# Performance work log

Hardware: AMD Instinct MI355X
Metric: run time of the kernel (lower is better)

## Reference

```python
import jax, jax.numpy as jnp
from jax import lax
import numpy as np

M, CLS, K, DL, DC, DO, BD = 87, 65, 128, 128, 128, 2048, 256
B, H, W = 256, 7, 7


def _c1(x, Wt, b):
    # 1x1 Conv2d: [B,Cin,H,W] -> [B,Cout,H,W]
    return jnp.einsum('oc,bchw->bohw', Wt, x) + b[None, :, None, None]


def _pagerank(edge, v_init, p=0.85, iters=100):
    # torch: transition = adj / adj.sum(dim=1)  (broadcast divides COLUMNS by row-sums)
    n = edge.shape[0]
    Wpr = p * edge / jnp.sum(edge, axis=1)[None, :]
    s = v_init * n                                  # [B,n,1]
    coef = (1.0 - p) / n
    def body(i, xv):
        zx = coef * jnp.sum(xv, axis=1, keepdims=True)      # z_T @ x -> [B,1,1]
        return jnp.einsum('ij,bjo->bio', Wpr, xv) + s * zx
    xv = lax.fori_loop(0, iters, body, s)
    nrm = jnp.sqrt(jnp.sum(xv * xv, axis=1, keepdims=True))  # F.normalize(dim=1)
    xv = xv / jnp.maximum(nrm, 1e-12)
    return (v_init + xv).reshape(v_init.shape[0], -1)        # [B,n]


def setup_inputs() -> dict:
    key = jax.random.key(0)
    ks = jax.random.split(key, 24)
    def w(k, shape, s=0.02):
        return jax.random.normal(k, shape, jnp.float32) * s
    rng = np.random.default_rng(0)
    A = (rng.random((M, M)) < 0.08).astype(np.float32)
    A = np.maximum(A, A.T)
    np.fill_diagonal(A, 1.0)   # symmetric adjacency with self-loops (degrees > 0)
    return {
        'x': jax.random.normal(ks[0], (B, DO, H, W), jnp.float32),
        'Wb': w(ks[1], (BD, DO)), 'bb': w(ks[2], (BD,), 0.01),
        'Wfc': w(ks[3], (CLS, BD)), 'Wfc2': w(ks[4], (CLS, BD)),
        'Wo1': w(ks[5], (4 * DL, DO)), 'bo1': w(ks[6], (4 * DL,), 0.01),
        'Wo2': w(ks[7], (DL, 4 * DL)), 'bo2': w(ks[8], (DL,), 0.01),
        'Wa': w(ks[9], (M, DL)), 'ba': w(ks[10], (M,), 0.01),
        'Wps': w(ks[11], (DC, DL)), 'bps': w(ks[12], (DC,), 0.01),
        'node_p': jax.random.uniform(ks[13], (K, M), jnp.float32, -0.1, 0.1),
        'Wg': w(ks[14], (DC, DC + K)), 'bg': w(ks[15], (DC,), 0.01),
        'Wsp': w(ks[16], (DL, DC)), 'bsp': w(ks[17], (DL,), 0.01),
        'Ws': w(ks[18], (1, DC + DL)), 'bs': w(ks[19], (1,), 0.01),
        'Wox1': w(ks[20], (4 * DL, DL)), 'box1': w(ks[21], (4 * DL,), 0.01),
        'Wox2': w(ks[22], (DO, 4 * DL)), 'box2': w(ks[23], (DO,), 0.01),
        'edge': jnp.asarray(A),
    }


def reference(x, Wb, bb, Wfc, Wfc2, Wo1, bo1, Wo2, bo2, Wa, ba, Wps, bps,
              node_p, Wg, bg, Wsp, bsp, Ws, bs, Wox1, box1, Wox2, box2, edge):
    Bsz, _, hl, wl = x.shape
    HW = hl * wl

    # global pooled branch
    x_p = jnp.mean(x, axis=(2, 3))                           # [B,2048]
    features_p = x_p @ Wb.T + bb                             # [B,256]
    pre_output = features_p @ Wfc.T                          # [B,65]
    pre_score = jax.nn.softmax(lax.stop_gradient(pre_output), axis=1)

    # personalized pagerank over the semantic graph (constant wrt grads)
    v_init = jnp.concatenate(
        [jnp.zeros((Bsz, M - CLS), x.dtype), pre_score], axis=1)[:, :, None]
    v_y = lax.stop_gradient(_pagerank(edge, v_init))         # [B,87]

    # local feature reduction 2048 -> 512 -> 128
    x_l = _c1(_c1(x, Wo1, bo1), Wo2, bo2)                    # [B,128,7,7]

    a = _c1(x_l, Wa, ba).reshape(Bsz, M, HW).transpose(0, 2, 1)   # [B,HW,87]
    ps = _c1(x_l, Wps, bps).reshape(Bsz, DC, HW)                  # [B,128,HW]
    m1 = jax.nn.relu(jnp.matmul(ps, a))                           # [B,128,87]

    # replicate torch's exact (k, B*m) reshape + flat v_y broadcast
    node = jnp.broadcast_to(node_p[None], (Bsz, K, M)).reshape(K, Bsz * M)
    node = (v_y.reshape(-1) * node).reshape(Bsz, K, M)

    g = jnp.einsum('oc,bcm->bom', Wg, jnp.concatenate([node, m1], axis=1)) \
        + bg[None, :, None]                                   # [B,128,87]

    # D^-1/2 A D^-1/2 graph propagation
    Dinv = jnp.sum(edge, axis=0) ** -0.5
    edge_norm = Dinv[:, None] * edge * Dinv[None, :]
    m2 = jax.nn.relu(jnp.einsum('bcm,mn->bcn', g, edge_norm))  # [B,128,87]

    sp = jnp.einsum('oc,bcm->bom', Wsp, m2) + bsp[None, :, None]  # [B,128,87]

    # conv_s over concat(m2_expand, x_expand) is separable: avoid the
    # [B,256,HW,87] tensor entirely (1 output channel, 1x1 kernel).
    Ws1, Ws2 = Ws[0, :DC], Ws[0, DC:]
    t_node = jnp.einsum('c,bcm->bm', Ws1, m2)                  # [B,87]
    t_pix = jnp.einsum('c,bcp->bp', Ws2, x_l.reshape(Bsz, DL, HW))  # [B,HW]
    s_logits = t_node[:, :, None] + t_pix[:, None, :] + bs[0]  # [B,87,HW]
    s_att = jax.nn.softmax(s_logits, axis=1)                   # softmax over nodes

    m3 = jax.nn.relu(jnp.matmul(sp, s_att)).reshape(Bsz, DL, hl, wl)
    m3 = _c1(_c1(m3, Wox1, box1), Wox2, box2)                  # [B,2048,7,7]

    feature_aug = jnp.mean(m3, axis=(2, 3)) @ Wb.T + bb
    features = features_p + feature_aug
    outputs2 = features @ Wfc2.T
    softmax_outputs = jax.nn.softmax(outputs2, axis=1)
    return (features, outputs2, softmax_outputs, pre_output, features_p)
```

## Files before the change

### kernel.cpp

```cpp
#include <hip/hip_runtime.h>
#include <cmath>


typedef __attribute__((ext_vector_type(8))) short short8;
typedef __attribute__((ext_vector_type(4))) short s16x4;
typedef __attribute__((ext_vector_type(4))) float f32x4;

constexpr size_t OFF_W12BF = 0;
constexpr size_t OFF_T1BF  = 131072;
constexpr size_t OFF_WBBF  = 262144;
constexpr size_t OFF_XPBF  = 524288;
constexpr size_t OFF_WAPBF = 786432;
constexpr size_t OFF_WG2BF = 800768;
constexpr size_t OFF_ENPBF = 808960;
constexpr size_t OFF_B215  = 813568;
constexpr size_t OFF_B12   = 813792;
constexpr size_t OFF_WPR   = 813920;
constexpr size_t OFF_BTMP  = 821496;
constexpr size_t OFF_WC    = 823544;
constexpr size_t OFF_BC    = 856312;
constexpr size_t OFF_VY    = 856568;
constexpr size_t OFF_NT    = 878848;
constexpr size_t OFF_PART  = 901376;

__device__ __forceinline__ unsigned short f2bf(float f) {
  unsigned u = __builtin_bit_cast(unsigned, f);
  u += 0x7fffu + ((u >> 16) & 1u);
  return (unsigned short)(u >> 16);
}
__device__ __forceinline__ float bf2f(unsigned short s) {
  return __builtin_bit_cast(float, ((unsigned)s) << 16);
}

__global__ __launch_bounds__(256) void ksetup_all(
    const float* __restrict__ Wb,  const float* __restrict__ bb,
    const float* __restrict__ Wa,  const float* __restrict__ ba,
    const float* __restrict__ Wps, const float* __restrict__ bps,
    const float* __restrict__ Wg,  const float* __restrict__ edge,
    const float* __restrict__ Wo2, const float* __restrict__ Wo1,
    const float* __restrict__ Wox2,const float* __restrict__ Wox1,
    const float* __restrict__ box1,const float* __restrict__ box2,
    const float* __restrict__ bo1, const float* __restrict__ bo2,
    float* __restrict__ ws, float* __restrict__ featp)
{
  __shared__ alignas(16) short As[64*72];
  __shared__ alignas(16) short Bs[64*72];
  int blk = blockIdx.x, tid = threadIdx.x;
  if (blk < 2048) {
    int idx = blk*256 + tid;
    ((unsigned short*)(ws+OFF_WBBF))[idx] = f2bf(Wb[idx]);
  } else if (blk < 2304) {
    int idx = (blk-2048)*256 + tid;
    featp[idx] = bb[idx & 255];
  } else if (blk < 2432) {
    int idx = (blk-2304)*256 + tid;
    ws[OFF_WC + idx] = 0.f;
  } else if (blk < 2544) {
    int idx = (blk-2432)*256 + tid;
    int r = idx >> 7, c = idx & 127;
    float v;
    if (r < 128)      v = Wps[r*128 + c];
    else if (r < 215) v = Wa[(r-128)*128 + c];
    else              v = 0.f;
    ((unsigned short*)(ws+OFF_WAPBF))[idx] = f2bf(v);
  } else if (blk < 2608) {
    int idx = (blk-2544)*256 + tid;
    int o = idx >> 7, d = idx & 127;
    ((unsigned short*)(ws+OFF_WG2BF))[idx] = f2bf(Wg[o*256 + 128 + d]);
  } else if (blk < 2644) {
    int idx = (blk-2608)*256 + tid;
    int m = idx / 96, n = idx % 96;
    float v = 0.f;
    if (m < 87 && n < 87) {
      float sm = 0.f, sn = 0.f;
      for (int k = 0; k < 87; ++k) { sm += edge[k*87+m]; sn += edge[k*87+n]; }
      v = edge[m*87+n] / sqrtf(sm*sn);
    }
    ((unsigned short*)(ws+OFF_ENPBF))[idx] = f2bf(v);
  } else if (blk < 2674) {
    int idx = (blk-2644)*256 + tid;
    if (idx < 87*87) {
      int j = idx % 87;
      float rs = 0.f;
      for (int k = 0; k < 87; ++k) rs += edge[j*87+k];
      ws[OFF_WPR + idx] = 0.85f * edge[idx] / rs;
    }
  } else if (blk == 2674) {
    if (tid < 224) {
      float v = (tid < 128) ? bps[tid] : (tid < 215 ? ba[tid-128] : 0.f);
      ws[OFF_B215 + tid] = v;
    }
  } else if (blk < 2803) {
    int gb = blk - 2675;
    const float *A, *B; unsigned short* C; int lda, ldb, ldc, i0, j0;
    if (gb < 64) {
      A = Wo2; B = Wo1; C = (unsigned short*)(ws+OFF_W12BF);
      lda = 512; ldb = 2048; ldc = 2048;
      i0 = (gb & 1)*64; j0 = (gb >> 1)*64;
    } else {
      int b2 = gb - 64;
      A = Wox2; B = Wox1; C = (unsigned short*)(ws+OFF_T1BF);
      lda = 512; ldb = 128; ldc = 128;
      i0 = (b2 >> 1)*64; j0 = (b2 & 1)*64;
    }
    int w = tid >> 6, l = tid & 63, quad = l >> 4, lane16 = l & 15;
    f32x4 acc[4];
    #pragma unroll
    for (int i = 0; i < 4; ++i) acc[i] = (f32x4)(0.f);
    for (int kc = 0; kc < 512; kc += 64) {
      for (int t = tid; t < 1024; t += 256) {
        int r = t >> 4, k4 = t & 15;
        float4 v = *(const float4*)&A[(size_t)(i0+r)*lda + kc + k4*4];
        s16x4 sv; sv[0]=(short)f2bf(v.x); sv[1]=(short)f2bf(v.y); sv[2]=(short)f2bf(v.z); sv[3]=(short)f2bf(v.w);
        *(s16x4*)&As[r*72 + k4*4] = sv;
      }
      for (int t = tid; t < 1024; t += 256) {
        int kr = t >> 4, n4 = t & 15;
        float4 v = *(const float4*)&B[(size_t)(kc+kr)*ldb + j0 + n4*4];
        Bs[(n4*4+0)*72 + kr] = (short)f2bf(v.x);
        Bs[(n4*4+1)*72 + kr] = (short)f2bf(v.y);
        Bs[(n4*4+2)*72 + kr] = (short)f2bf(v.z);
        Bs[(n4*4+3)*72 + kr] = (short)f2bf(v.w);
      }
      __syncthreads();
      #pragma unroll
      for (int ks = 0; ks < 2; ++ks) {
        short8 a = *(const short8*)&As[(w*16+lane16)*72 + ks*32 + quad*8];
        #pragma unroll
        for (int nt = 0; nt < 4; ++nt) {
          short8 b8 = *(const short8*)&Bs[(nt*16+lane16)*72 + ks*32 + quad*8];
          acc[nt] = __builtin_amdgcn_mfma_f32_16x16x32_bf16(a, b8, acc[nt], 0, 0, 0);
        }
      }
      __syncthreads();
    }
    #pragma unroll
    for (int nt = 0; nt < 4; ++nt)
      #pragma unroll
      for (int r = 0; r < 4; ++r)
        C[(size_t)(i0 + w*16 + quad*4 + r)*ldc + j0 + nt*16 + lane16] = f2bf(acc[nt][r]);
  } else {
    int vb = blk - 2803;
    int w = tid >> 6, l = tid & 63;
    if (vb < 512) {
      int o = vb*4 + w;
      float s = 0.f;
      for (int h = l; h < 512; h += 64) s += Wox2[(size_t)o*512 + h] * box1[h];
      for (int off = 32; off; off >>= 1) s += __shfl_down(s, off, 64);
      if (l == 0) ws[OFF_BTMP + o] = s + box2[o];
    } else {
      int o = (vb - 512)*4 + w;
      float s = 0.f;
      for (int h = l; h < 512; h += 64) s += Wo2[(size_t)o*512 + h] * bo1[h];
      for (int off = 32; off; off >>= 1) s += __shfl_down(s, off, 64);
      if (l == 0) ws[OFF_B12 + o] = s + bo2[o];
    }
  }
}

__global__ __launch_bounds__(512, 6) void kmain5(const float* __restrict__ x,
                                                 const short* __restrict__ w12bf,
                                                 short* __restrict__ xpbf,
                                                 float* __restrict__ part)
{
  __shared__ alignas(16) short Bt[2][64*72];
  int b = blockIdx.x, q = blockIdx.y, tid = threadIdx.x;
  int w = tid >> 6, l = tid & 63;
  int quad = l >> 4, lane16 = l & 15;
  const float* xb = x + ((size_t)b*2048 + q*512)*49;

  int p4A = tid % 13, cA = tid / 13;
  int tB = tid + 512;
  int p4B = tB % 13, cB = tB / 13;
  bool hasB = (tid < 320);

  float fA[4], fB[4];
  {
    if (p4A < 12) {
      float4 v = *(const float4*)(xb + cA*49 + p4A*4);
      fA[0]=v.x; fA[1]=v.y; fA[2]=v.z; fA[3]=v.w;
    } else fA[0] = xb[cA*49 + 48];
    if (hasB) {
      if (p4B < 12) {
        float4 v = *(const float4*)(xb + cB*49 + p4B*4);
        fB[0]=v.x; fB[1]=v.y; fB[2]=v.z; fB[3]=v.w;
      } else fB[0] = xb[cB*49 + 48];
    }
  }

  f32x4 acc[4];
  #pragma unroll
  for (int i = 0; i < 4; ++i) acc[i] = (f32x4)(0.f);

  for (int kci = 0; kci < 8; ++kci) {
    short* bt = Bt[kci & 1];
    if (p4A < 12) {
      #pragma unroll
      for (int i = 0; i < 4; ++i) bt[(p4A*4+i)*72 + cA] = (short)f2bf(fA[i]);
    } else bt[48*72 + cA] = (short)f2bf(fA[0]);
    if (hasB) {
      if (p4B < 12) {
        #pragma unroll
        for (int i = 0; i < 4; ++i) bt[(p4B*4+i)*72 + cB] = (short)f2bf(fB[i]);
      } else bt[48*72 + cB] = (short)f2bf(fB[0]);
    }
    __syncthreads();
    if (kci < 7) {
      const float* xc = xb + (size_t)(kci+1)*64*49;
      if (p4A < 12) {
        float4 v = *(const float4*)(xc + cA*49 + p4A*4);
        fA[0]=v.x; fA[1]=v.y; fA[2]=v.z; fA[3]=v.w;
      } else fA[0] = xc[cA*49 + 48];
      if (hasB) {
        if (p4B < 12) {
          float4 v = *(const float4*)(xc + cB*49 + p4B*4);
          fB[0]=v.x; fB[1]=v.y; fB[2]=v.z; fB[3]=v.w;
        } else fB[0] = xc[cB*49 + 48];
      }
    }
    const short* wr = w12bf + (size_t)(w*16 + lane16)*2048 + q*512 + kci*64 + quad*8;
    short8 a0 = *(const short8*)(wr);
    short8 a1 = *(const short8*)(wr + 32);
    #pragma unroll
    for (int ni = 0; ni < 4; ++ni) {
      const short* br = bt + (ni*16 + lane16)*72 + quad*8;
      short8 b0 = *(const short8*)(br);
      short8 b1 = *(const short8*)(br + 32);
      acc[ni] = __builtin_amdgcn_mfma_f32_16x16x32_bf16(a0, b0, acc[ni], 0, 0, 0);
      acc[ni] = __builtin_amdgcn_mfma_f32_16x16x32_bf16(a1, b1, acc[ni], 0, 0, 0);
    }
    if (tid < 64) {
      float s = 0.f;
      for (int p = 0; p < 49; ++p)
        s += bf2f((unsigned short)bt[p*72 + tid]);
      xpbf[(size_t)b*2048 + q*512 + kci*64 + tid] = (short)f2bf(s * (1.f/49.f));
    }
  }
  float* po = part + ((size_t)q*256 + b)*6656;
  #pragma unroll
  for (int ni = 0; ni < 4; ++ni) {
    int p = ni*16 + lane16;
    if (p < 49) {
      #pragma unroll
      for (int r = 0; r < 4; ++r) {
        int o = w*16 + quad*4 + r;
        po[o*52 + p] = acc[ni][r];
      }
    }
  }
}

__global__ __launch_bounds__(256) void kwcf(const float* __restrict__ Wb,
                                            const float* __restrict__ bb,
                                            const short* __restrict__ xpbf,
                                            float* __restrict__ featp,
                                            float* __restrict__ ws)
{
  __shared__ alignas(16) short As[64*72];
  __shared__ alignas(16) short Bs[64*72];
  int blk = blockIdx.x, tid = threadIdx.x;
  if (blk < 64) {
    const short* wbbf = (const short*)(ws+OFF_WBBF);
    const short* t1s  = (const short*)(ws+OFF_T1BF);
    int i0 = (blk & 3)*64, j0 = ((blk >> 2) & 1)*64, kc0 = (blk >> 3)*256;
    int w = tid >> 6, l = tid & 63, quad = l >> 4, lane16 = l & 15;
    f32x4 acc[4];
    #pragma unroll
    for (int i = 0; i < 4; ++i) acc[i] = (f32x4)(0.f);
    for (int kc = kc0; kc < kc0+256; kc += 64) {
      for (int t = tid; t < 512; t += 256) {
        int r = t >> 3, c8 = t & 7;
        *(short8*)&As[r*72 + c8*8] = *(const short8*)&wbbf[(size_t)(i0+r)*2048 + kc + c8*8];
      }
      for (int t = tid; t < 1024; t += 256) {
        int kr = t >> 4, n4 = t & 15;
        s16x4 v = *(const s16x4*)&t1s[(size_t)(kc+kr)*128 + j0 + n4*4];
        Bs[(n4*4+0)*72 + kr] = v[0];
        Bs[(n4*4+1)*72 + kr] = v[1];
        Bs[(n4*4+2)*72 + kr] = v[2];
        Bs[(n4*4+3)*72 + kr] = v[3];
      }
      __syncthreads();
      #pragma unroll
      for (int ks = 0; ks < 2; ++ks) {
        short8 a = *(const short8*)&As[(w*16+lane16)*72 + ks*32 + quad*8];
        #pragma unroll
        for (int nt = 0; nt < 4; ++nt) {
          short8 b8 = *(const short8*)&Bs[(nt*16+lane16)*72 + ks*32 + quad*8];
          acc[nt] = __builtin_amdgcn_mfma_f32_16x16x32_bf16(a, b8, acc[nt], 0, 0, 0);
        }
      }
      __syncthreads();
    }
    #pragma unroll
    for (int nt = 0; nt < 4; ++nt)
      #pragma unroll
      for (int r = 0; r < 4; ++r)
        atomicAdd(&ws[OFF_WC + (size_t)(i0 + w*16 + quad*4 + r)*128 + j0 + nt*16 + lane16], acc[nt][r]);
  } else if (blk < 128) {
    int j = (blk-64)*4 + (tid >> 6), l = tid & 63;
    float s = 0.f;
    for (int c = l; c < 2048; c += 64) s += Wb[(size_t)j*2048 + c] * ws[OFF_BTMP + c];
    for (int off = 32; off; off >>= 1) s += __shfl_down(s, off, 64);
    if (l == 0) ws[OFF_BC + j] = s + bb[j];
  } else {
    const short* wbbf = (const short*)(ws+OFF_WBBF);
    int idx = blk - 128;
    int i0 = (idx & 3)*64, j0 = ((idx >> 2) & 3)*64, kc0 = (idx >> 4)*256;
    int w = tid >> 6, l = tid & 63, quad = l >> 4, lane16 = l & 15;
    f32x4 acc[4];
    #pragma unroll
    for (int i = 0; i < 4; ++i) acc[i] = (f32x4)(0.f);
    for (int kc = kc0; kc < kc0+256; kc += 32) {
      short8 a = *(const short8*)&xpbf[(size_t)(i0 + w*16 + lane16)*2048 + kc + quad*8];
      #pragma unroll
      for (int nt = 0; nt < 4; ++nt) {
        short8 b8 = *(const short8*)&wbbf[(size_t)(j0 + nt*16 + lane16)*2048 + kc + quad*8];
        acc[nt] = __builtin_amdgcn_mfma_f32_16x16x32_bf16(a, b8, acc[nt], 0, 0, 0);
      }
    }
    #pragma unroll
    for (int nt = 0; nt < 4; ++nt)
      #pragma unroll
      for (int r = 0; r < 4; ++r)
        atomicAdd(&featp[(size_t)(i0 + w*16 + quad*4 + r)*256 + j0 + nt*16 + lane16], acc[nt][r]);
  }
}

__global__ __launch_bounds__(128, 1) void kpr(const float* __restrict__ featp,
                                              const float* __restrict__ Wfc,
                                              const float* __restrict__ wpr,
                                              float* __restrict__ preo,
                                              float* __restrict__ vy)
{
  __shared__ alignas(16) float fpr[256];
  __shared__ alignas(16) float po[68];
  __shared__ alignas(16) float vs[2][88];
  __shared__ float red[2];
  int b = blockIdx.x, tid = threadIdx.x;
  fpr[tid] = featp[b*256 + tid];
  fpr[tid+128] = featp[b*256 + 128 + tid];
  __syncthreads();
  if (tid < 65) {
    float s = 0.f;
    for (int c = 0; c < 256; c += 4) {
      float4 w4 = *(const float4*)&Wfc[tid*256 + c];
      s += w4.x*fpr[c] + w4.y*fpr[c+1] + w4.z*fpr[c+2] + w4.w*fpr[c+3];
    }
    po[tid] = s;
    preo[b*65 + tid] = s;
  }
  __syncthreads();
  if (tid < 64) {
    float v = po[tid];
    if (tid == 0) v = fmaxf(v, po[64]);
    float mx = v;
    #pragma unroll
    for (int off = 32; off; off >>= 1) mx = fmaxf(mx, __shfl_down(mx, off, 64));
    mx = __shfl(mx, 0, 64);
    float e = expf(po[tid]-mx) + ((tid == 0) ? expf(po[64]-mx) : 0.f);
    float sm = e;
    #pragma unroll
    for (int off = 32; off; off >>= 1) sm += __shfl_down(sm, off, 64);
    if (tid == 0) { red[0] = mx; red[1] = 1.f/sm; }
  }
  __syncthreads();
  float vinit = 0.f;
  if (tid >= 22 && tid < 87) vinit = expf(po[tid-22]-red[0]) * red[1];
  float s_i = vinit * 87.f;
  float wrow[87];
  if (tid < 87) {
    float add = s_i * (0.15f/87.0f);
    #pragma unroll
    for (int j = 0; j < 87; ++j) wrow[j] = wpr[tid*87 + j] + add;
    vs[0][tid] = s_i;
  }
  __syncthreads();
  for (int it = 0; it < 64; ++it) {
    const float* vc = vs[it & 1];
    if (tid < 87) {
      float nv = 0.f;
      #pragma unroll
      for (int j4 = 0; j4 < 21; ++j4) {
        float4 v4 = *(const float4*)&vc[j4*4];
        nv += wrow[j4*4+0]*v4.x + wrow[j4*4+1]*v4.y + wrow[j4*4+2]*v4.z + wrow[j4*4+3]*v4.w;
      }
      nv += wrow[84]*vc[84] + wrow[85]*vc[85] + wrow[86]*vc[86];
      vs[(it+1) & 1][tid] = nv;
    }
    __syncthreads();
  }
  if (tid < 64) {
    float v = vs[0][tid]*vs[0][tid];
    if (tid < 23) v += vs[0][64+tid]*vs[0][64+tid];
    #pragma unroll
    for (int off = 32; off; off >>= 1) v += __shfl_down(v, off, 64);
    if (tid == 0) red[0] = 1.f / fmaxf(sqrtf(v), 1e-12f);
  }
  __syncthreads();
  if (tid < 87) vy[b*87 + tid] = vinit + vs[0][tid]*red[0];
}

__global__ __launch_bounds__(256) void knode(const float* __restrict__ Wg,
                                             const float* __restrict__ node_p,
                                             const float* __restrict__ vy,
                                             float* __restrict__ nt)
{
  int idx = blockIdx.x*256 + threadIdx.x;
  int par = idx / 11264;
  int r = idx % 11264;
  int o = r / 88, m = r % 88;
  float v = 0.f;
  if (m < 87) {
    float s = 0.f;
    for (int k = 0; k < 128; ++k)
      s += Wg[o*256+k] * node_p[k*87+m] * vy[(par*128+k)*87+m];
    v = s;
  }
  nt[idx] = v;
}

__global__ __launch_bounds__(512) void kgraph_all(
    const float* __restrict__ part,  const float* __restrict__ b12,
    const short* __restrict__ wapbf, const float* __restrict__ b215,
    const short* __restrict__ wg2bf, const float* __restrict__ nt,
    const float* __restrict__ bg,    const short* __restrict__ enpbf,
    const float* __restrict__ Wsp,   const float* __restrict__ bsp,
    const float* __restrict__ Ws,    const float* __restrict__ wc,
    const float* __restrict__ bc,    const float* __restrict__ featp,
    const float* __restrict__ Wfc2,
    float* __restrict__ feat, float* __restrict__ out2, float* __restrict__ soft)
{
  extern __shared__ char smraw[];
  short* XT = (short*)smraw;
  short* At = XT + 8704;
  short* M1 = At + 16128;
  short* G  = M1 + 13056;
  short* M2 = G  + 13312;
  float* fb  = (float*)(M2 + 13312);
  float* wsm = fb;
  float* tnb = fb + 96;
  float* zs  = fb + 192;
  float* m3s = fb + 320;
  float* fs  = fb + 448;
  float* o2s = fb + 704;
  float* red = fb + 776;

  int b = blockIdx.x, tid = threadIdx.x;
  int w = tid >> 6, l = tid & 63, quad = l >> 4, lane16 = l & 15;

  const float* p0 = part + (size_t)b*6656;
  const float* p1 = p0 + (size_t)256*6656;
  const float* p2 = p1 + (size_t)256*6656;
  const float* p3 = p2 + (size_t)256*6656;
  for (int t = tid; t < 6656; t += 512) {
    int o = t / 52, p = t % 52;
    XT[p*136 + o] = (short)f2bf(p0[t] + p1[t] + p2[t] + p3[t] + b12[o]);
  }
  for (int t = tid; t < 1536; t += 512) {
    int p = 52 + t/128, o = t % 128;
    XT[p*136 + o] = 0;
  }
  __syncthreads();

  for (int t = w; t < 56; t += 8) {
    int mt = t >> 2, n4 = t & 3;
    f32x4 acc = (f32x4)(0.f);
    #pragma unroll
    for (int ks = 0; ks < 4; ++ks) {
      short8 a  = *(const short8*)&wapbf[(size_t)(mt*16+lane16)*128 + ks*32 + quad*8];
      short8 b8 = *(const short8*)&XT[(n4*16+lane16)*136 + ks*32 + quad*8];
      acc = __builtin_amdgcn_mfma_f32_16x16x32_bf16(a, b8, acc, 0, 0, 0);
    }
    int p = n4*16 + lane16;
    #pragma unroll
    for (int r = 0; r < 4; ++r) {
      int rr = mt*16 + quad*4 + r;
      At[rr*72 + p] = (p < 49) ? (short)f2bf(acc[r] + b215[rr]) : (short)0;
    }
  }
  __syncthreads();

  for (int t = w; t < 48; t += 8) {
    int mt = t / 8, n4 = t % 8;
    f32x4 acc = (f32x4)(0.f);
    #pragma unroll
    for (int ks = 0; ks < 2; ++ks) {
      short8 a  = *(const short8*)&At[(128 + mt*16 + lane16)*72 + ks*32 + quad*8];
      short8 b8 = *(const short8*)&At[(n4*16+lane16)*72 + ks*32 + quad*8];
      acc = __builtin_amdgcn_mfma_f32_16x16x32_bf16(a, b8, acc, 0, 0, 0);
    }
    int d = n4*16 + lane16;
    #pragma unroll
    for (int r = 0; r < 4; ++r) {
      int m = mt*16 + quad*4 + r;
      M1[m*136 + d] = (short)f2bf(fmaxf(acc[r], 0.f));
    }
  }
  __syncthreads();

  const float* ntb = nt + (size_t)(b & 1)*11264;
  for (int t = w; t < 48; t += 8) {
    int mt = t / 6, n4 = t % 6;
    f32x4 acc = (f32x4)(0.f);
    #pragma unroll
    for (int ks = 0; ks < 4; ++ks) {
      short8 a  = *(const short8*)&wg2bf[(size_t)(mt*16+lane16)*128 + ks*32 + quad*8];
      short8 b8 = *(const short8*)&M1[(n4*16+lane16)*136 + ks*32 + quad*8];
      acc = __builtin_amdgcn_mfma_f32_16x16x32_bf16(a, b8, acc, 0, 0, 0);
    }
    int m = n4*16 + lane16;
    #pragma unroll
    for (int r = 0; r < 4; ++r) {
      int o = mt*16 + quad*4 + r;
      float v = acc[r] + bg[o] + ((m < 88) ? ntb[o*88 + m] : 0.f);
      G[o*104 + m] = (short)f2bf(v);
    }
  }
  __syncthreads();

  for (int t = w; t < 48; t += 8) {
    int mt = t / 6, n4 = t % 6;
    f32x4 acc = (f32x4)(0.f);
    #pragma unroll
    for (int ks = 0; ks < 3; ++ks) {
      short8 a  = *(const short8*)&G[(mt*16+lane16)*104 + ks*32 + quad*8];
      short8 b8 = *(const short8*)&enpbf[(size_t)(n4*16+lane16)*96 + ks*32 + quad*8];
      acc = __builtin_amdgcn_mfma_f32_16x16x32_bf16(a, b8, acc, 0, 0, 0);
    }
    int n = n4*16 + lane16;
    #pragma unroll
    for (int r = 0; r < 4; ++r) {
      int c = mt*16 + quad*4 + r;
      M2[c*104 + n] = (short)f2bf(fmaxf(acc[r], 0.f));
    }
  }
  __syncthreads();

  if (tid < 87) {
    float s = 0.f;
    for (int c = 0; c < 128; ++c) s += Ws[c] * bf2f((unsigned short)M2[c*104 + tid]);
    tnb[tid] = s;
  }
  __syncthreads();
  if (tid < 64) {
    float v = tnb[tid];
    if (tid < 23) v = fmaxf(v, tnb[64+tid]);
    float mx = v;
    #pragma unroll
    for (int off = 32; off; off >>= 1) mx = fmaxf(mx, __shfl_down(mx, off, 64));
    mx = __shfl(mx, 0, 64);
    float e0 = expf(tnb[tid]-mx);
    float e1 = (tid < 23) ? expf(tnb[64+tid]-mx) : 0.f;
    float sm = e0 + e1;
    #pragma unroll
    for (int off = 32; off; off >>= 1) sm += __shfl_down(sm, off, 64);
    sm = __shfl(sm, 0, 64);
    float inv = 1.f/sm;
    wsm[tid] = e0*inv;
    if (tid < 23) wsm[64+tid] = e1*inv;
  }
  __syncthreads();
  if (tid < 128) {
    float s = 0.f;
    for (int m = 0; m < 87; ++m) s += bf2f((unsigned short)M2[tid*104 + m]) * wsm[m];
    zs[tid] = s;
  }
  __syncthreads();
  if (tid < 128) {
    float s = 0.f;
    for (int c = 0; c < 128; ++c) s += Wsp[tid*128 + c] * zs[c];
    m3s[tid] = fmaxf(s + bsp[tid], 0.f);
  }
  __syncthreads();

  if (tid < 256) {
    float s = 0.f;
    #pragma unroll 4
    for (int d4 = 0; d4 < 32; ++d4) {
      float4 w4 = *(const float4*)&wc[tid*128 + d4*4];
      s += w4.x*m3s[d4*4] + w4.y*m3s[d4*4+1] + w4.z*m3s[d4*4+2] + w4.w*m3s[d4*4+3];
    }
    float f = featp[b*256 + tid] + bc[tid] + s;
    fs[tid] = f;
    feat[b*256 + tid] = f;
  }
  __syncthreads();
  if (tid < 65) {
    float s = 0.f;
    for (int j = 0; j < 256; ++j) s += Wfc2[tid*256 + j] * fs[j];
    out2[b*65 + tid] = s;
    o2s[tid] = s;
  }
  __syncthreads();
  if (tid < 64) {
    float v = o2s[tid];
    if (tid == 0) v = fmaxf(v, o2s[64]);
    float mx = v;
    #pragma unroll
    for (int off = 32; off; off >>= 1) mx = fmaxf(mx, __shfl_down(mx, off, 64));
    mx = __shfl(mx, 0, 64);
    float e = expf(o2s[tid]-mx) + ((tid == 0) ? expf(o2s[64]-mx) : 0.f);
    float sm = e;
    #pragma unroll
    for (int off = 32; off; off >>= 1) sm += __shfl_down(sm, off, 64);
    if (tid == 0) { red[0] = mx; red[1] = 1.f/sm; }
  }
  __syncthreads();
  if (tid < 65) soft[b*65 + tid] = expf(o2s[tid]-red[0]) * red[1];
}

extern "C" void kernel_launch(void* const* d_in, const int* in_sizes, int n_in,
                              void* d_out, int out_size, void* d_ws, size_t ws_size,
                              hipStream_t stream)
{
  (void)in_sizes; (void)n_in; (void)out_size; (void)ws_size;
  const float* x      = (const float*)d_in[0];
  const float* Wb     = (const float*)d_in[1];
  const float* bb     = (const float*)d_in[2];
  const float* Wfc    = (const float*)d_in[3];
  const float* Wfc2   = (const float*)d_in[4];
  const float* Wo1    = (const float*)d_in[5];
  const float* bo1    = (const float*)d_in[6];
  const float* Wo2    = (const float*)d_in[7];
  const float* bo2    = (const float*)d_in[8];
  const float* Wa     = (const float*)d_in[9];
  const float* ba     = (const float*)d_in[10];
  const float* Wps    = (const float*)d_in[11];
  const float* bps    = (const float*)d_in[12];
  const float* node_p = (const float*)d_in[13];
  const float* Wg     = (const float*)d_in[14];
  const float* bg     = (const float*)d_in[15];
  const float* Wsp    = (const float*)d_in[16];
  const float* bsp    = (const float*)d_in[17];
  const float* Ws     = (const float*)d_in[18];
  const float* Wox1   = (const float*)d_in[20];
  const float* box1   = (const float*)d_in[21];
  const float* Wox2   = (const float*)d_in[22];
  const float* box2   = (const float*)d_in[23];
  const float* edge   = (const float*)d_in[24];

  float* ws   = (float*)d_ws;
  float* out  = (float*)d_out;
  float* feat  = out;
  float* out2  = out + 65536;
  float* soft  = out + 82176;
  float* preo  = out + 98816;
  float* featp = out + 115456;

  ksetup_all<<<3347, 256, 0, stream>>>(Wb, bb, Wa, ba, Wps, bps, Wg, edge,
                                       Wo2, Wo1, Wox2, Wox1, box1, box2, bo1, bo2,
                                       ws, featp);
  kmain5<<<dim3(256,4), 512, 0, stream>>>(x, (const short*)(ws + OFF_W12BF),
                                          (short*)(ws + OFF_XPBF), ws + OFF_PART);
  kwcf<<<256, 256, 0, stream>>>(Wb, bb, (const short*)(ws + OFF_XPBF), featp, ws);
  kpr<<<256, 128, 0, stream>>>(featp, Wfc, ws + OFF_WPR, preo, ws + OFF_VY);
  knode<<<88, 256, 0, stream>>>(Wg, node_p, ws + OFF_VY, ws + OFF_NT);
  kgraph_all<<<256, 512, 132144, stream>>>(ws + OFF_PART, ws + OFF_B12,
                                           (const short*)(ws + OFF_WAPBF),
                                           ws + OFF_B215,
                                           (const short*)(ws + OFF_WG2BF),
                                           ws + OFF_NT, bg,
                                           (const short*)(ws + OFF_ENPBF),
                                           Wsp, bsp, Ws,
                                           ws + OFF_WC, ws + OFF_BC, featp, Wfc2,
                                           feat, out2, soft);
}
```

Before: 363.0 us.

## Split serial dot products across four lanes with shuffle reductions

```diff
diff --git a/kernel.cpp b/kernel.cpp
--- a/kernel.cpp
+++ b/kernel.cpp
@@ -327,28 +327,33 @@
   }
 }
 
-__global__ __launch_bounds__(128, 1) void kpr(const float* __restrict__ featp,
-                                              const float* __restrict__ Wfc,
-                                              const float* __restrict__ wpr,
-                                              float* __restrict__ preo,
-                                              float* __restrict__ vy)
+__global__ __launch_bounds__(384) void kpr(const float* __restrict__ featp,
+                                           const float* __restrict__ Wfc,
+                                           const float* __restrict__ wpr,
+                                           float* __restrict__ preo,
+                                           float* __restrict__ vy)
 {
   __shared__ alignas(16) float fpr[256];
   __shared__ alignas(16) float po[68];
-  __shared__ alignas(16) float vs[2][88];
-  __shared__ float red[2];
+  __shared__ alignas(16) float vsA[88];
+  __shared__ alignas(16) float vsB[88];
+  __shared__ alignas(16) float vis[88];
+  __shared__ float rd[4];
   int b = blockIdx.x, tid = threadIdx.x;
-  fpr[tid] = featp[b*256 + tid];
-  fpr[tid+128] = featp[b*256 + 128 + tid];
-  __syncthreads();
-  if (tid < 65) {
+  if (tid < 256) fpr[tid] = featp[b*256 + tid];
+  __syncthreads();
+  if (tid < 260) {
+    int row = tid >> 2, p = tid & 3;
     float s = 0.f;
-    for (int c = 0; c < 256; c += 4) {
-      float4 w4 = *(const float4*)&Wfc[tid*256 + c];
-      s += w4.x*fpr[c] + w4.y*fpr[c+1] + w4.z*fpr[c+2] + w4.w*fpr[c+3];
-    }
-    po[tid] = s;
-    preo[b*65 + tid] = s;
+    const float* wr = Wfc + row*256 + p*64;
+    #pragma unroll
+    for (int c = 0; c < 64; c += 4) {
+      float4 w4 = *(const float4*)&wr[c];
+      s += w4.x*fpr[p*64+c] + w4.y*fpr[p*64+c+1] + w4.z*fpr[p*64+c+2] + w4.w*fpr[p*64+c+3];
+    }
+    s += __shfl_xor(s, 1, 64);
+    s += __shfl_xor(s, 2, 64);
+    if (p == 0) { po[row] = s; preo[b*65 + row] = s; }
   }
   __syncthreads();
   if (tid < 64) {
@@ -362,62 +367,71 @@
     float sm = e;
     #pragma unroll
     for (int off = 32; off; off >>= 1) sm += __shfl_down(sm, off, 64);
-    if (tid == 0) { red[0] = mx; red[1] = 1.f/sm; }
-  }
-  __syncthreads();
-  float vinit = 0.f;
-  if (tid >= 22 && tid < 87) vinit = expf(po[tid-22]-red[0]) * red[1];
-  float s_i = vinit * 87.f;
-  float wrow[87];
-  if (tid < 87) {
-    float add = s_i * (0.15f/87.0f);
-    #pragma unroll
-    for (int j = 0; j < 87; ++j) wrow[j] = wpr[tid*87 + j] + add;
-    vs[0][tid] = s_i;
-  }
-  __syncthreads();
+    if (tid == 0) { rd[0] = mx; rd[1] = 1.f/sm; }
+  }
+  __syncthreads();
+  if (tid < 88) {
+    float vin = (tid >= 22 && tid < 87) ? expf(po[tid-22]-rd[0])*rd[1] : 0.f;
+    vis[tid] = vin;
+    vsA[tid] = vin * 87.f;
+    vsB[tid] = 0.f;
+  }
+  __syncthreads();
+  float wrow[22];
+  const int m4 = tid >> 2, pp = tid & 3;
+  if (tid < 348) {
+    float add = vis[m4] * 0.15f;
+    #pragma unroll
+    for (int jj = 0; jj < 22; ++jj) {
+      int j = pp*22 + jj;
+      wrow[jj] = (j < 87) ? (wpr[m4*87 + j] + add) : 0.f;
+    }
+  }
   for (int it = 0; it < 64; ++it) {
-    const float* vc = vs[it & 1];
-    if (tid < 87) {
+    const float* vc = (it & 1) ? vsB : vsA;
+    float* vn = (it & 1) ? vsA : vsB;
+    if (tid < 348) {
       float nv = 0.f;
       #pragma unroll
-      for (int j4 = 0; j4 < 21; ++j4) {
-        float4 v4 = *(const float4*)&vc[j4*4];
-        nv += wrow[j4*4+0]*v4.x + wrow[j4*4+1]*v4.y + wrow[j4*4+2]*v4.z + wrow[j4*4+3]*v4.w;
-      }
-      nv += wrow[84]*vc[84] + wrow[85]*vc[85] + wrow[86]*vc[86];
-      vs[(it+1) & 1][tid] = nv;
+      for (int jj = 0; jj < 22; ++jj) nv += wrow[jj] * vc[pp*22 + jj];
+      nv += __shfl_xor(nv, 1, 64);
+      nv += __shfl_xor(nv, 2, 64);
+      if (pp == 0) vn[m4] = nv;
     }
     __syncthreads();
   }
   if (tid < 64) {
-    float v = vs[0][tid]*vs[0][tid];
-    if (tid < 23) v += vs[0][64+tid]*vs[0][64+tid];
+    float v = vsA[tid]*vsA[tid];
+    if (tid < 23) v += vsA[64+tid]*vsA[64+tid];
     #pragma unroll
     for (int off = 32; off; off >>= 1) v += __shfl_down(v, off, 64);
-    if (tid == 0) red[0] = 1.f / fmaxf(sqrtf(v), 1e-12f);
-  }
-  __syncthreads();
-  if (tid < 87) vy[b*87 + tid] = vinit + vs[0][tid]*red[0];
-}
-
-__global__ __launch_bounds__(256) void knode(const float* __restrict__ Wg,
+    if (tid == 0) rd[2] = 1.f / fmaxf(sqrtf(v), 1e-12f);
+  }
+  __syncthreads();
+  if (tid < 87) vy[b*87 + tid] = vis[tid] + vsA[tid]*rd[2];
+}
+
+__global__ __launch_bounds__(384) void knode(const float* __restrict__ Wg,
                                              const float* __restrict__ node_p,
                                              const float* __restrict__ vy,
                                              float* __restrict__ nt)
 {
-  int idx = blockIdx.x*256 + threadIdx.x;
-  int par = idx / 11264;
-  int r = idx % 11264;
+  int tid = threadIdx.x;
+  if (tid >= 352) return;
+  int out = blockIdx.x*88 + (tid >> 2);
+  int par = out / 11264;
+  int r = out % 11264;
   int o = r / 88, m = r % 88;
-  float v = 0.f;
+  int p = tid & 3;
+  float s = 0.f;
   if (m < 87) {
-    float s = 0.f;
-    for (int k = 0; k < 128; ++k)
-      s += Wg[o*256+k] * node_p[k*87+m] * vy[(par*128+k)*87+m];
-    v = s;
-  }
-  nt[idx] = v;
+    const float* vrow = vy + (size_t)(par*128)*87 + m;
+    for (int k = p*32; k < p*32+32; ++k)
+      s += Wg[o*256 + k] * node_p[k*87 + m] * vrow[k*87];
+  }
+  s += __shfl_xor(s, 1, 64);
+  s += __shfl_xor(s, 2, 64);
+  if (p == 0) nt[out] = s;
 }
 
 __global__ __launch_bounds__(512) void kgraph_all(
@@ -537,10 +551,14 @@
   }
   __syncthreads();
 
-  if (tid < 87) {
+  if (tid < 348) {
+    int m = tid >> 2, p = tid & 3;
     float s = 0.f;
-    for (int c = 0; c < 128; ++c) s += Ws[c] * bf2f((unsigned short)M2[c*104 + tid]);
-    tnb[tid] = s;
+    for (int c = p*32; c < p*32+32; ++c)
+      s += Ws[c] * bf2f((unsigned short)M2[c*104 + m]);
+    s += __shfl_xor(s, 1, 64);
+    s += __shfl_xor(s, 2, 64);
+    if (p == 0) tnb[m] = s;
   }
   __syncthreads();
   if (tid < 64) {
@@ -561,16 +579,23 @@
     if (tid < 23) wsm[64+tid] = e1*inv;
   }
   __syncthreads();
-  if (tid < 128) {
+  {
+    int c = tid >> 2, p = tid & 3;
     float s = 0.f;
-    for (int m = 0; m < 87; ++m) s += bf2f((unsigned short)M2[tid*104 + m]) * wsm[m];
-    zs[tid] = s;
-  }
-  __syncthreads();
-  if (tid < 128) {
+    for (int mm = p*22; mm < p*22+22 && mm < 87; ++mm)
+      s += bf2f((unsigned short)M2[c*104 + mm]) * wsm[mm];
+    s += __shfl_xor(s, 1, 64);
+    s += __shfl_xor(s, 2, 64);
+    if (p == 0) zs[c] = s;
+  }
+  __syncthreads();
+  {
+    int d = tid >> 2, p = tid & 3;
     float s = 0.f;
-    for (int c = 0; c < 128; ++c) s += Wsp[tid*128 + c] * zs[c];
-    m3s[tid] = fmaxf(s + bsp[tid], 0.f);
+    for (int c = p*32; c < p*32+32; ++c) s += Wsp[d*128 + c] * zs[c];
+    s += __shfl_xor(s, 1, 64);
+    s += __shfl_xor(s, 2, 64);
+    if (p == 0) m3s[d] = fmaxf(s + bsp[d], 0.f);
   }
   __syncthreads();
 
@@ -586,11 +611,16 @@
     feat[b*256 + tid] = f;
   }
   __syncthreads();
-  if (tid < 65) {
+  if (tid < 260) {
+    int row = tid >> 2, p = tid & 3;
     float s = 0.f;
-    for (int j = 0; j < 256; ++j) s += Wfc2[tid*256 + j] * fs[j];
-    out2[b*65 + tid] = s;
-    o2s[tid] = s;
+    for (int c = p*64; c < p*64+64; c += 4) {
+      float4 w4 = *(const float4*)&Wfc2[row*256 + c];
+      s += w4.x*fs[c] + w4.y*fs[c+1] + w4.z*fs[c+2] + w4.w*fs[c+3];
+    }
+    s += __shfl_xor(s, 1, 64);
+    s += __shfl_xor(s, 2, 64);
+    if (p == 0) { out2[b*65 + row] = s; o2s[row] = s; }
   }
   __syncthreads();
   if (tid < 64) {
@@ -654,8 +684,8 @@
   kmain5<<<dim3(256,4), 512, 0, stream>>>(x, (const short*)(ws + OFF_W12BF),
                                           (short*)(ws + OFF_XPBF), ws + OFF_PART);
   kwcf<<<256, 256, 0, stream>>>(Wb, bb, (const short*)(ws + OFF_XPBF), featp, ws);
-  kpr<<<256, 128, 0, stream>>>(featp, Wfc, ws + OFF_WPR, preo, ws + OFF_VY);
-  knode<<<88, 256, 0, stream>>>(Wg, node_p, ws + OFF_VY, ws + OFF_NT);
+  kpr<<<256, 384, 0, stream>>>(featp, Wfc, ws + OFF_WPR, preo, ws + OFF_VY);
+  knode<<<256, 384, 0, stream>>>(Wg, node_p, ws + OFF_VY, ws + OFF_NT);
   kgraph_all<<<256, 512, 132144, stream>>>(ws + OFF_PART, ws + OFF_B12,
                                            (const short*)(ws + OFF_WAPBF),
                                            ws + OFF_B215,
```

Measured after the change: 331.1 us. -8.8%, faster.
